# Optimization experiments

Hardware: AMD Instinct MI355X
Metric: run time of the kernel (lower is better)

The kernel has to match this reference:

```python
import jax, jax.numpy as jnp
import numpy as np

I3 = jnp.eye(3, dtype=jnp.float32)
G_VEC = jnp.array([0.0, 0.0, -9.80665], dtype=jnp.float32)
# Q diag: [cov_omega x3, cov_acc x3, cov_b_omega x3, cov_b_acc x3, cov_Rot_c_i x3, cov_t_c_i x3]
Q_DIAG = jnp.array([1e-3] * 3 + [1e-2] * 3 + [6e-9] * 3 + [2e-4] * 3 + [1e-9] * 3 + [1e-9] * 3, dtype=jnp.float32)
N_NORM_ROT = 100
N_NORM_ROT_CI = 1000


def skew(v):
    z = jnp.zeros_like(v[0])
    return jnp.stack([jnp.stack([z, -v[2], v[1]]),
                      jnp.stack([v[2], z, -v[0]]),
                      jnp.stack([-v[1], v[0], z])])


def so3exp(phi):
    a2 = jnp.sum(phi * phi)
    small = a2 < 1e-12
    a = jnp.sqrt(jnp.where(small, 1.0, a2))
    axis = phi / a
    c, s = jnp.cos(a), jnp.sin(a)
    big = c * I3 + (1.0 - c) * jnp.outer(axis, axis) + s * skew(axis)
    return jnp.where(small, I3 + skew(phi), big)


def sen3exp(xi):
    # SE_2(3) exponential: xi[:3]=rotation, xi[3:9]=(v, p) parts
    phi = xi[:3]
    a2 = jnp.sum(phi * phi)
    small = a2 < 1e-12
    a = jnp.sqrt(jnp.where(small, 1.0, a2))
    axis = phi / a
    c, s = jnp.cos(a), jnp.sin(a)
    sk = skew(axis)
    R = jnp.where(small, I3 + skew(phi),
                  c * I3 + (1.0 - c) * jnp.outer(axis, axis) + s * sk)
    J = jnp.where(small, I3 + 0.5 * skew(phi),
                  (s / a) * I3 + (1.0 - s / a) * jnp.outer(axis, axis) + ((1.0 - c) / a) * sk)
    x = J @ xi[3:].reshape(2, 3).T  # (3,2): columns are dv, dp
    return R, x


def normalize_rot(R):
    # Polar-factor re-orthonormalization (equivalent to the SVD-based
    # normalize_rot for near-rotation matrices), via Newton-Schulz iteration
    # which is smooth and jit/vjp friendly.
    def body(X, _):
        return 1.5 * X - 0.5 * (X @ X.T @ X), None
    X, _ = jax.lax.scan(body, R, None, length=8)
    return X


def from_rpy(roll, pitch, yaw):
    cr, sr = jnp.cos(roll), jnp.sin(roll)
    cp, sp = jnp.cos(pitch), jnp.sin(pitch)
    cy, sy = jnp.cos(yaw), jnp.sin(yaw)
    one = jnp.ones_like(cr)
    zero = jnp.zeros_like(cr)
    Rx = jnp.stack([jnp.stack([one, zero, zero]), jnp.stack([zero, cr, -sr]), jnp.stack([zero, sr, cr])])
    Ry = jnp.stack([jnp.stack([cp, zero, sp]), jnp.stack([zero, one, zero]), jnp.stack([-sp, zero, cp])])
    Rz = jnp.stack([jnp.stack([cy, -sy, zero]), jnp.stack([sy, cy, zero]), jnp.stack([zero, zero, one])])
    return Rz @ Ry @ Rx


def init_covariance():
    P = jnp.zeros((21, 21), dtype=jnp.float32)
    P = P.at[:2, :2].set(1e-3 * jnp.eye(2))     # cov_Rot0 (no yaw error)
    P = P.at[3:5, 3:5].set(0.1 * jnp.eye(2))    # cov_v0
    P = P.at[9:12, 9:12].set(6e-3 * I3)         # cov_b_omega0
    P = P.at[12:15, 12:15].set(4e-3 * I3)       # cov_b_acc0
    P = P.at[15:18, 15:18].set(1e-6 * I3)       # cov_Rot_c_i0
    P = P.at[18:21, 18:21].set(5e-3 * I3)       # cov_t_c_i0
    return P


def propagate_cov(P, Rot, v, p, dt):
    F = jnp.zeros((21, 21), dtype=P.dtype)
    F = F.at[3:6, :3].set(skew(G_VEC))
    F = F.at[6:9, 3:6].set(I3)
    F = F.at[:3, 9:12].set(-Rot)
    F = F.at[3:6, 9:12].set(-skew(v) @ Rot)
    F = F.at[3:6, 12:15].set(-Rot)
    F = F.at[6:9, 9:12].set(-skew(p) @ Rot)
    G = jnp.zeros((21, 18), dtype=P.dtype)
    G = G.at[:3, :3].set(Rot)
    G = G.at[3:6, 3:6].set(Rot)
    G = G.at[9:12, 6:9].set(I3)
    G = G.at[12:15, 9:12].set(I3)
    G = G.at[15:18, 12:15].set(I3)
    G = G.at[18:21, 15:18].set(I3)
    F = F * dt
    G = G * dt
    F2 = F @ F
    Phi = jnp.eye(21, dtype=P.dtype) + F + 0.5 * F2 + (F2 @ F) / 6.0  # 3rd-order expm
    return Phi @ (P + (G * Q_DIAG[None, :]) @ G.T) @ Phi.T


def _step(carry, xs):
    Rot, v, p, b_om, b_ac, Rci, tci, P = carry
    u_i, dt_i, mcov_i, i = xs
    # ---- propagate ----
    acc = Rot @ (u_i[3:6] - b_ac) + G_VEC
    v_n = v + acc * dt_i
    p_n = p + v * dt_i + 0.5 * acc * dt_i * dt_i
    Rot_n = Rot @ so3exp((u_i[:3] - b_om) * dt_i)
    P_n = propagate_cov(P, Rot, v, p, dt_i)
    # ---- update: zero lateral/vertical body-velocity pseudo-measurement ----
    omega = u_i[:3] - b_om
    Rot_body = Rot_n @ Rci
    v_imu = Rot_n.T @ v_n
    v_body = Rci.T @ v_imu + skew(tci) @ omega
    H = jnp.zeros((2, 21), dtype=P.dtype)
    H = H.at[:, 3:6].set(Rot_body.T[1:])
    H = H.at[:, 15:18].set((Rci.T @ skew(v_imu))[1:])
    H = H.at[:, 9:12].set(skew(tci)[1:])
    H = H.at[:, 18:21].set(-skew(omega)[1:])
    r = -v_body[1:]
    Rm = jnp.diag(mcov_i)
    S = H @ P_n @ H.T + Rm                    # (2,2)
    K = jnp.linalg.solve(S, H @ P_n).T        # K = P H^T S^-1 (P, S symmetric)
    dx = K @ r                                 # (21,)
    dR, dxi = sen3exp(dx[:9])
    Rot_u = dR @ Rot_n
    v_u = dR @ v_n + dxi[:, 0]
    p_u = dR @ p_n + dxi[:, 1]
    b_om_u = b_om + dx[9:12]
    b_ac_u = b_ac + dx[12:15]
    Rci_u = so3exp(dx[15:18]) @ Rci
    tci_u = tci + dx[18:21]
    IKH = jnp.eye(21, dtype=P.dtype) - K @ H
    P_u = IKH @ P_n @ IKH.T + K @ Rm @ K.T    # Joseph form
    P_u = 0.5 * (P_u + P_u.T)
    Rot_u = jnp.where(i % N_NORM_ROT == 0, normalize_rot(Rot_u), Rot_u)
    Rci_u = jnp.where(i % N_NORM_ROT_CI == 0, normalize_rot(Rci_u), Rci_u)
    carry = (Rot_u, v_u, p_u, b_om_u, b_ac_u, Rci_u, tci_u, P_u)
    return carry, (Rot_u, v_u, p_u, b_om_u, b_ac_u, Rci_u, tci_u)


def _forward(t, u, measurements_covs, v_mes, p_mes, ang0, N):
    dt = t[1:N] - t[:N - 1]
    Rot0 = from_rpy(ang0[0], ang0[1], ang0[2])
    z3 = jnp.zeros(3, dtype=u.dtype)
    carry0 = (Rot0, v_mes[0], z3, z3, z3, I3, z3, init_covariance())
    xs = (u[1:N], dt, measurements_covs[1:N], jnp.arange(1, N))
    _, ys = jax.lax.scan(_step, carry0, xs)
    Rot = jnp.concatenate([Rot0[None], ys[0]], axis=0)
    v = jnp.concatenate([v_mes[0][None], ys[1]], axis=0)
    p = jnp.concatenate([z3[None], ys[2]], axis=0)
    b_omega = jnp.concatenate([z3[None], ys[3]], axis=0)
    b_acc = jnp.concatenate([z3[None], ys[4]], axis=0)
    Rot_c_i = jnp.concatenate([I3[None], ys[5]], axis=0)
    t_c_i = jnp.concatenate([z3[None], ys[6]], axis=0)
    return (Rot, v, p, b_omega, b_acc, Rot_c_i, t_c_i)


def setup_inputs() -> dict:
    key = jax.random.key(0)
    N = 20000  # 200 s at 100 Hz IMU
    k0, k1, k2, k3, k4, k5 = jax.random.split(key, 6)
    t = jnp.arange(N, dtype=jnp.float32) * 0.01
    gyro = 0.01 * jax.random.normal(k0, (N, 3), dtype=jnp.float32)
    acc = jnp.array([0.0, 0.0, 9.80665], jnp.float32) + 0.1 * jax.random.normal(k1, (N, 3), dtype=jnp.float32)
    u = jnp.concatenate([gyro, acc], axis=1)
    measurements_covs = 0.1 + jax.random.uniform(k2, (N, 2), dtype=jnp.float32)
    v_mes = jax.random.normal(k3, (N, 3), dtype=jnp.float32)
    p_mes = jax.random.normal(k4, (N, 3), dtype=jnp.float32)
    ang0 = 0.01 * jax.random.normal(k5, (3,), dtype=jnp.float32)
    return dict(t=t, u=u, measurements_covs=measurements_covs, v_mes=v_mes, p_mes=p_mes, ang0=ang0, N=N)


def reference(t, u, measurements_covs, v_mes, p_mes, ang0, N):
    return _forward(t, u, measurements_covs, v_mes, p_mes, ang0, N)
```

## Files before the change

kernel.cpp:

```cpp
#include <hip/hip_runtime.h>

#define GRAV 9.80665f

__device__ __forceinline__ float sel3(int r, float a0, float a1, float a2){
  float x = (r==1)? a1 : a0;
  return (r>=2)? a2 : x;
}

__device__ __forceinline__ void mm33(float* __restrict__ O, const float* A, const float* B){
#pragma unroll
  for(int r=0;r<3;++r){
#pragma unroll
    for(int c=0;c<3;++c){
      O[r*3+c] = A[r*3+0]*B[0*3+c] + A[r*3+1]*B[1*3+c] + A[r*3+2]*B[2*3+c];
    }
  }
}

__device__ __forceinline__ void rot_from_t2(float t_, float p0, float p1, float p2, float* R){
  float c_, k1_, k2_;
  if (t_ < 1e-4f){
    c_  = 1.f - t_*(0.5f - t_*((1.f/24.f) - t_*(1.f/720.f)));
    k2_ = 1.f - t_*((1.f/6.f) - t_*((1.f/120.f) - t_*(1.f/5040.f)));
    k1_ = 0.5f - t_*((1.f/24.f) - t_*(1.f/720.f));
  } else {
    float a = sqrtf(t_);
    c_ = __cosf(a);
    float s = __sinf(a);
    k2_ = s/a;
    k1_ = (1.f - c_)/t_;
  }
  R[0]=c_+k1_*p0*p0;      R[1]=k1_*p0*p1-k2_*p2;  R[2]=k1_*p0*p2+k2_*p1;
  R[3]=k1_*p0*p1+k2_*p2;  R[4]=c_+k1_*p1*p1;      R[5]=k1_*p1*p2-k2_*p0;
  R[6]=k1_*p0*p2-k2_*p1;  R[7]=k1_*p1*p2+k2_*p0;  R[8]=c_+k1_*p2*p2;
}

__device__ __forceinline__ void normalize_rot9(float* X){
#pragma unroll 1
  for(int it=0; it<8; ++it){
    float Y[9], Z[9];
#pragma unroll
    for(int r=0;r<3;++r)
#pragma unroll
      for(int c=0;c<3;++c)
        Y[r*3+c] = X[r*3+0]*X[c*3+0] + X[r*3+1]*X[c*3+1] + X[r*3+2]*X[c*3+2];
#pragma unroll
    for(int r=0;r<3;++r)
#pragma unroll
      for(int c=0;c<3;++c)
        Z[r*3+c] = Y[r*3+0]*X[0*3+c] + Y[r*3+1]*X[1*3+c] + Y[r*3+2]*X[2*3+c];
#pragma unroll
    for(int e=0;e<9;++e) X[e] = 1.5f*X[e] - 0.5f*Z[e];
  }
}

__device__ __forceinline__ float pick_state(int l,
    const float* Rt, const float* vv, const float* pp,
    const float* bw, const float* ba, const float* Rc, const float* tc){
  float s = Rt[0];
  s=(l==1)?Rt[1]:s;  s=(l==2)?Rt[2]:s;  s=(l==3)?Rt[3]:s;  s=(l==4)?Rt[4]:s;
  s=(l==5)?Rt[5]:s;  s=(l==6)?Rt[6]:s;  s=(l==7)?Rt[7]:s;  s=(l==8)?Rt[8]:s;
  s=(l==9)?vv[0]:s;  s=(l==10)?vv[1]:s; s=(l==11)?vv[2]:s;
  s=(l==12)?pp[0]:s; s=(l==13)?pp[1]:s; s=(l==14)?pp[2]:s;
  s=(l==15)?bw[0]:s; s=(l==16)?bw[1]:s; s=(l==17)?bw[2]:s;
  s=(l==18)?ba[0]:s; s=(l==19)?ba[1]:s; s=(l==20)?ba[2]:s;
  s=(l==21)?Rc[0]:s; s=(l==22)?Rc[1]:s; s=(l==23)?Rc[2]:s;
  s=(l==24)?Rc[3]:s; s=(l==25)?Rc[4]:s; s=(l==26)?Rc[5]:s;
  s=(l==27)?Rc[6]:s; s=(l==28)?Rc[7]:s; s=(l==29)?Rc[8]:s;
  s=(l==30)?tc[0]:s; s=(l==31)?tc[1]:s; s=(l==32)?tc[2]:s;
  return s;
}

__global__ __launch_bounds__(64,1)
void iekf_scan_kernel(const float* __restrict__ t,
                      const float* __restrict__ u,
                      const float* __restrict__ mcov,
                      const float* __restrict__ v_mes,
                      const float* __restrict__ ang0,
                      float* __restrict__ out, int N)
{
  const int l = threadIdx.x;
  __shared__ float Pm[441];
  __shared__ float Eb[441];
  __shared__ float PnS[441];
  __shared__ float PuS[441];
  __shared__ float HPs[42];
  __shared__ float Ks[42];
  __shared__ float Ws[42];
  __shared__ float dxs[21];

  float Rt[9], vv[3], pp[3], bw[3], ba[3], Rc[9], tc[3];
  {
    float rl = ang0[0], pt = ang0[1], yw = ang0[2];
    float cr=cosf(rl), sr=sinf(rl), cp=cosf(pt), sp=sinf(pt), cy=cosf(yw), sy=sinf(yw);
    Rt[0]=cy*cp; Rt[1]=cy*sp*sr - sy*cr; Rt[2]=cy*sp*cr + sy*sr;
    Rt[3]=sy*cp; Rt[4]=sy*sp*sr + cy*cr; Rt[5]=sy*sp*cr - cy*sr;
    Rt[6]=-sp;   Rt[7]=cp*sr;            Rt[8]=cp*cr;
  }
  vv[0]=v_mes[0]; vv[1]=v_mes[1]; vv[2]=v_mes[2];
#pragma unroll
  for(int k=0;k<3;++k){ pp[k]=0.f; bw[k]=0.f; ba[k]=0.f; tc[k]=0.f; }
  Rc[0]=1.f;Rc[1]=0.f;Rc[2]=0.f;Rc[3]=0.f;Rc[4]=1.f;Rc[5]=0.f;Rc[6]=0.f;Rc[7]=0.f;Rc[8]=1.f;

  for (int e=l; e<441; e+=64){
    int r=e/21, c=e-(e/21)*21;
    float vI=0.f;
    if (r==c){
      if (r<2) vI=0.001f;
      else if (r==3||r==4) vI=0.1f;
      else if (r>=9&&r<12) vI=0.006f;
      else if (r>=12&&r<15) vI=0.004f;
      else if (r>=15&&r<18) vI=1e-6f;
      else if (r>=18) vI=0.005f;
    }
    Pm[e]=vI;
  }

  int ostr=0; float* op = out;
  {
    int obase=0, ooff=0;
    if (l<9)       {obase=0;    ostr=9; ooff=l;}
    else if (l<12) {obase=9*N;  ostr=3; ooff=l-9;}
    else if (l<15) {obase=12*N; ostr=3; ooff=l-12;}
    else if (l<18) {obase=15*N; ostr=3; ooff=l-15;}
    else if (l<21) {obase=18*N; ostr=3; ooff=l-18;}
    else if (l<30) {obase=21*N; ostr=9; ooff=l-21;}
    else           {obase=30*N; ostr=3; ooff=l-30;}
    op = out + obase + ooff;
  }

  int idxA=0, rrA=0, ccA=0; float qvA=0.f; bool rrtA=false;
  if (l<9)      { rrA=l/3; ccA=l-rrA*3; idxA=rrA*21+ccA; qvA=0.001f; rrtA=true; }
  else if (l<18){ int m=l-9; rrA=m/3; ccA=m-rrA*3; idxA=(3+rrA)*21+(3+ccA); qvA=0.01f; rrtA=true; }
  else if (l<30){ int j=l-18; int b=j/3, d=j-b*3; int row=9+b*3+d; idxA=row*21+row;
                  qvA = (b==0)?6e-9f : (b==1)?2e-4f : 1e-9f; }

  const int g21 = l/21;
  const int c21 = l - g21*21;

  static const int cols[12] = {3,4,5, 9,10,11, 15,16,17, 18,19,20};

  {
    float sv = pick_state(l, Rt, vv, pp, bw, ba, Rc, tc);
    if (l<33) op[0] = sv;
  }
  __syncthreads();

  float tA = t[0], tB = t[1];
  float cu[6];
#pragma unroll
  for(int k=0;k<6;++k) cu[k]=u[6+k];
  float cm0=mcov[2], cm1=mcov[3];

  int nx100=100, nx1000=1000;

#pragma unroll 1
  for (int i=1; i<N; ++i){
    float dt = tB - tA;
    float u0=cu[0], u1=cu[1], u2=cu[2], u3=cu[3], u4=cu[4], u5=cu[5];
    float crm0=cm0, crm1=cm1;
    if (i+1 < N){
      tA = tB; tB = t[i+1];
#pragma unroll
      for(int k=0;k<6;++k) cu[k]=u[(i+1)*6+k];
      cm0 = mcov[(i+1)*2]; cm1 = mcov[(i+1)*2+1];
    }
    float dt2=dt*dt, gdt=GRAV*dt, hdt=0.5f*dt, g6=gdt*dt*(1.0f/6.0f), hdt2=0.5f*dt*dt;

    float w0=u0-bw[0], w1=u1-bw[1], w2=u2-bw[2];
    float aa0=u3-ba[0], aa1=u4-ba[1], aa2=u5-ba[2];
    float acc0 = Rt[0]*aa0+Rt[1]*aa1+Rt[2]*aa2;
    float acc1 = Rt[3]*aa0+Rt[4]*aa1+Rt[5]*aa2;
    float acc2 = Rt[6]*aa0+Rt[7]*aa1+Rt[8]*aa2 - GRAV;
    float vn0=vv[0]+acc0*dt, vn1=vv[1]+acc1*dt, vn2=vv[2]+acc2*dt;
    float pn0=pp[0]+vv[0]*dt+acc0*hdt2;
    float pn1=pp[1]+vv[1]*dt+acc1*hdt2;
    float pn2=pp[2]+vv[2]*dt+acc2*hdt2;
    float ph0=w0*dt, ph1=w1*dt, ph2=w2*dt;
    float dRs[9]; rot_from_t2(ph0*ph0+ph1*ph1+ph2*ph2, ph0,ph1,ph2, dRs);
    float Rn[9]; mm33(Rn, Rt, dRs);
    float Rb[9]; mm33(Rb, Rn, Rc);
    float vi0 = Rn[0]*vn0+Rn[3]*vn1+Rn[6]*vn2;
    float vi1 = Rn[1]*vn0+Rn[4]*vn1+Rn[7]*vn2;
    float vi2 = Rn[2]*vn0+Rn[5]*vn1+Rn[8]*vn2;
    float vb1 = Rc[1]*vi0+Rc[4]*vi1+Rc[7]*vi2 + (tc[2]*w0 - tc[0]*w2);
    float vb2 = Rc[2]*vi0+Rc[5]*vi1+Rc[8]*vi2 + (tc[0]*w1 - tc[1]*w0);
    float rr0 = -vb1, rr1 = -vb2;

    float H0[12], H1[12];
    H0[0]=Rb[1]; H0[1]=Rb[4]; H0[2]=Rb[7];
    H1[0]=Rb[2]; H1[1]=Rb[5]; H1[2]=Rb[8];
    H0[3]=tc[2];  H0[4]=0.f;   H0[5]=-tc[0];
    H1[3]=-tc[1]; H1[4]=tc[0]; H1[5]=0.f;
    H0[6]=Rc[4]*vi2 - Rc[7]*vi1;  H0[7]=Rc[7]*vi0 - Rc[1]*vi2;  H0[8]=Rc[1]*vi1 - Rc[4]*vi0;
    H1[6]=Rc[5]*vi2 - Rc[8]*vi1;  H1[7]=Rc[8]*vi0 - Rc[2]*vi2;  H1[8]=Rc[2]*vi1 - Rc[5]*vi0;
    H0[9]=-w2; H0[10]=0.f; H0[11]=w0;
    H1[9]=w1;  H1[10]=-w0; H1[11]=0.f;

    float Bm[9], Cab[9], D2a[9];
#pragma unroll
    for(int k=0;k<3;++k){
      float b0=-dt*Rt[k], b1=-dt*Rt[3+k], b2=-dt*Rt[6+k];
      float c0=dt*(vv[2]*Rt[3+k]-vv[1]*Rt[6+k]);
      float c1=dt*(vv[0]*Rt[6+k]-vv[2]*Rt[k]);
      float c2=dt*(vv[1]*Rt[k]-vv[0]*Rt[3+k]);
      float d0=dt*(pp[2]*Rt[3+k]-pp[1]*Rt[6+k]);
      float d1=dt*(pp[0]*Rt[6+k]-pp[2]*Rt[k]);
      float d2=dt*(pp[1]*Rt[k]-pp[0]*Rt[3+k]);
      Bm[k]=b0; Bm[3+k]=b1; Bm[6+k]=b2;
      Cab[k]=c0+0.5f*gdt*b1; Cab[3+k]=c1-0.5f*gdt*b0; Cab[6+k]=c2;
      D2a[k]=d0+hdt*c0+g6*b1; D2a[3+k]=d1+hdt*c1-g6*b0; D2a[6+k]=d2+hdt*c2;
    }
    float Bs0=sel3(g21,Bm[0],Bm[3],Bm[6]),  Bs1=sel3(g21,Bm[1],Bm[4],Bm[7]),  Bs2=sel3(g21,Bm[2],Bm[5],Bm[8]);
    float Cs0=sel3(g21,Cab[0],Cab[3],Cab[6]),Cs1=sel3(g21,Cab[1],Cab[4],Cab[7]),Cs2=sel3(g21,Cab[2],Cab[5],Cab[8]);
    float Ds0=sel3(g21,D2a[0],D2a[3],D2a[6]),Ds1=sel3(g21,D2a[1],D2a[4],D2a[7]),Ds2=sel3(g21,D2a[2],D2a[5],D2a[8]);

    if (l<30){
      float addv;
      if (rrtA){
        float ra0=sel3(rrA,Rt[0],Rt[3],Rt[6]), ra1=sel3(rrA,Rt[1],Rt[4],Rt[7]), ra2=sel3(rrA,Rt[2],Rt[5],Rt[8]);
        float rb0=sel3(ccA,Rt[0],Rt[3],Rt[6]), rb1=sel3(ccA,Rt[1],Rt[4],Rt[7]), rb2=sel3(ccA,Rt[2],Rt[5],Rt[8]);
        addv = qvA*dt2*(ra0*rb0+ra1*rb1+ra2*rb2);
      } else addv = qvA*dt2;
      Pm[idxA] += addv;
    }
    __syncthreads();

    if (l<63){
      int c = c21;
      float m0 = Pm[c], m1 = Pm[21+c];
      float mr = Pm[g21*21+c], m3r = Pm[(3+g21)*21+c], m6r = Pm[(6+g21)*21+c];
      float m9 =Pm[9*21+c],  m10=Pm[10*21+c], m11=Pm[11*21+c];
      float m12=Pm[12*21+c], m13=Pm[13*21+c], m14=Pm[14*21+c];
      float Ar = (g21==0)? gdt*m1 : (g21==1)? -gdt*m0 : 0.f;
      float bterm = Bs0*m12+Bs1*m13+Bs2*m14;
      float e0 = mr + Bs0*m9+Bs1*m10+Bs2*m11;
      float e1 = m3r + Ar + Cs0*m9+Cs1*m10+Cs2*m11 + bterm;
      float e2 = m6r + hdt*Ar + dt*m3r + Ds0*m9+Ds1*m10+Ds2*m11 + hdt*bterm;
      Eb[g21*21+c]=e0; Eb[(3+g21)*21+c]=e1; Eb[(6+g21)*21+c]=e2;
      int rw = 9+4*g21;
      Eb[rw*21+c]     = Pm[rw*21+c];
      Eb[(rw+1)*21+c] = Pm[(rw+1)*21+c];
      Eb[(rw+2)*21+c] = Pm[(rw+2)*21+c];
      Eb[(rw+3)*21+c] = Pm[(rw+3)*21+c];
    }
    __syncthreads();

    if (l<63){
      int r = c21;
      const float* Er = Eb + r*21;
      float e0a=Er[0], e1a=Er[1];
      float eg=Er[g21], e3g=Er[3+g21], e6g=Er[6+g21];
      float e9=Er[9],e10=Er[10],e11=Er[11],e12=Er[12],e13=Er[13],e14=Er[14];
      float Ag = (g21==0)? gdt*e1a : (g21==1)? -gdt*e0a : 0.f;
      float bterm = Bs0*e12+Bs1*e13+Bs2*e14;
      float q0 = eg + Bs0*e9+Bs1*e10+Bs2*e11;
      float q1 = e3g + Ag + Cs0*e9+Cs1*e10+Cs2*e11 + bterm;
      float q2 = e6g + hdt*Ag + dt*e3g + Ds0*e9+Ds1*e10+Ds2*e11 + hdt*bterm;
      PnS[r*21+g21]=q0; PnS[r*21+3+g21]=q1; PnS[r*21+6+g21]=q2;
      int cw = 9+4*g21;
      PnS[r*21+cw]=Er[cw]; PnS[r*21+cw+1]=Er[cw+1]; PnS[r*21+cw+2]=Er[cw+2]; PnS[r*21+cw+3]=Er[cw+3];
    }
    __syncthreads();

    if (l<42){
      int rH = l/21, c = l-(l/21)*21;
      float acc = 0.f;
#pragma unroll
      for(int k=0;k<12;++k){
        float h = (rH==0)? H0[k] : H1[k];
        acc += h * PnS[cols[k]*21 + c];
      }
      HPs[rH*21+c] = acc;
    }
    __syncthreads();

    float s00=crm0, s11=crm1, s01=0.f, s10=0.f;
#pragma unroll
    for(int k=0;k<12;++k){
      float hp0 = HPs[cols[k]];
      float hp1 = HPs[21+cols[k]];
      s00 += hp0*H0[k]; s01 += hp0*H1[k];
      s10 += hp1*H0[k]; s11 += hp1*H1[k];
    }
    float idet = 1.0f/(s00*s11 - s01*s10);
    float i00 =  s11*idet, i01 = -s01*idet, i10 = -s10*idet, i11 = s00*idet;
    if (l<21){
      float hp0=HPs[l], hp1=HPs[21+l];
      float K0 = i00*hp0 + i01*hp1;
      float K1 = i10*hp0 + i11*hp1;
      Ks[l*2]=K0; Ks[l*2+1]=K1;
      dxs[l] = K0*rr0 + K1*rr1;
    }
    __syncthreads();

    float dxr[21];
#pragma unroll
    for(int k=0;k<21;++k) dxr[k]=dxs[k];

    if (l<63){
      int c = c21;
      float hp0 = HPs[c], hp1 = HPs[21+c];
#pragma unroll
      for (int rrow=0; rrow<7; ++rrow){
        int r = g21*7+rrow;
        float k0=Ks[r*2], k1=Ks[r*2+1];
        PnS[r*21+c] -= k0*hp0 + k1*hp1;
      }
    }
    __syncthreads();

    if (l<42){
      int rW = l/21, ii = l-(l/21)*21;
      float acc=0.f;
#pragma unroll
      for(int k=0;k<12;++k){
        float h = (rW==0)? H0[k] : H1[k];
        acc += PnS[ii*21+cols[k]] * h;
      }
      Ws[ii*2+rW]=acc;
    }
    __syncthreads();

    if (l<63){
      int c = c21;
      float kc0=Ks[c*2], kc1=Ks[c*2+1];
#pragma unroll
      for(int rrow=0;rrow<7;++rrow){
        int r = g21*7+rrow;
        float w0_=Ws[r*2], w1_=Ws[r*2+1];
        float kr0=Ks[r*2], kr1=Ks[r*2+1];
        float tv=PnS[r*21+c];
        PuS[r*21+c] = tv - (w0_*kc0+w1_*kc1) + crm0*kr0*kc0 + crm1*kr1*kc1;
      }
    }
    __syncthreads();

    if (l<63){
      int c = c21;
#pragma unroll
      for(int rrow=0;rrow<7;++rrow){
        int r = g21*7+rrow;
        Pm[r*21+c] = 0.5f*(PuS[r*21+c] + PuS[c*21+r]);
      }
    }
    __syncthreads();

    float t2x = dxr[0]*dxr[0]+dxr[1]*dxr[1]+dxr[2]*dxr[2];
    float cX,k1X,k2X,j1X;
    if (t2x < 1e-4f){
      cX  = 1.f - t2x*(0.5f - t2x*((1.f/24.f) - t2x*(1.f/720.f)));
      k2X = 1.f - t2x*((1.f/6.f) - t2x*((1.f/120.f) - t2x*(1.f/5040.f)));
      k1X = 0.5f - t2x*((1.f/24.f) - t2x*(1.f/720.f));
      j1X = (1.f/6.f) - t2x*((1.f/120.f) - t2x*(1.f/5040.f));
    } else {
      float a = sqrtf(t2x);
      cX = __cosf(a);
      float s = __sinf(a);
      k2X = s/a; k1X = (1.f-cX)/t2x; j1X = (1.f-k2X)/t2x;
    }
    float dR[9];
    dR[0]=cX+k1X*dxr[0]*dxr[0];      dR[1]=k1X*dxr[0]*dxr[1]-k2X*dxr[2]; dR[2]=k1X*dxr[0]*dxr[2]+k2X*dxr[1];
    dR[3]=k1X*dxr[0]*dxr[1]+k2X*dxr[2]; dR[4]=cX+k1X*dxr[1]*dxr[1];      dR[5]=k1X*dxr[1]*dxr[2]-k2X*dxr[0];
    dR[6]=k1X*dxr[0]*dxr[2]-k2X*dxr[1]; dR[7]=k1X*dxr[1]*dxr[2]+k2X*dxr[0]; dR[8]=cX+k1X*dxr[2]*dxr[2];
    float Jm[9];
    Jm[0]=k2X+j1X*dxr[0]*dxr[0];      Jm[1]=j1X*dxr[0]*dxr[1]-k1X*dxr[2]; Jm[2]=j1X*dxr[0]*dxr[2]+k1X*dxr[1];
    Jm[3]=j1X*dxr[0]*dxr[1]+k1X*dxr[2]; Jm[4]=k2X+j1X*dxr[1]*dxr[1];      Jm[5]=j1X*dxr[1]*dxr[2]-k1X*dxr[0];
    Jm[6]=j1X*dxr[0]*dxr[2]-k1X*dxr[1]; Jm[7]=j1X*dxr[1]*dxr[2]+k1X*dxr[0]; Jm[8]=k2X+j1X*dxr[2]*dxr[2];

    float Ru[9]; mm33(Ru, dR, Rn);
    float vu0 = dR[0]*vn0+dR[1]*vn1+dR[2]*vn2 + Jm[0]*dxr[3]+Jm[1]*dxr[4]+Jm[2]*dxr[5];
    float vu1 = dR[3]*vn0+dR[4]*vn1+dR[5]*vn2 + Jm[3]*dxr[3]+Jm[4]*dxr[4]+Jm[5]*dxr[5];
    float vu2 = dR[6]*vn0+dR[7]*vn1+dR[8]*vn2 + Jm[6]*dxr[3]+Jm[7]*dxr[4]+Jm[8]*dxr[5];
    float pu0 = dR[0]*pn0+dR[1]*pn1+dR[2]*pn2 + Jm[0]*dxr[6]+Jm[1]*dxr[7]+Jm[2]*dxr[8];
    float pu1 = dR[3]*pn0+dR[4]*pn1+dR[5]*pn2 + Jm[3]*dxr[6]+Jm[4]*dxr[7]+Jm[5]*dxr[8];
    float pu2 = dR[6]*pn0+dR[7]*pn1+dR[8]*pn2 + Jm[6]*dxr[6]+Jm[7]*dxr[7]+Jm[8]*dxr[8];
    bw[0]+=dxr[9];  bw[1]+=dxr[10]; bw[2]+=dxr[11];
    ba[0]+=dxr[12]; ba[1]+=dxr[13]; ba[2]+=dxr[14];
    float Ec[9]; rot_from_t2(dxr[15]*dxr[15]+dxr[16]*dxr[16]+dxr[17]*dxr[17], dxr[15],dxr[16],dxr[17], Ec);
    float Rcu[9]; mm33(Rcu, Ec, Rc);
    tc[0]+=dxr[18]; tc[1]+=dxr[19]; tc[2]+=dxr[20];

    if (i==nx100){ normalize_rot9(Ru); nx100+=100; }
    if (i==nx1000){ normalize_rot9(Rcu); nx1000+=1000; }

#pragma unroll
    for(int k=0;k<9;++k){ Rt[k]=Ru[k]; Rc[k]=Rcu[k]; }
    vv[0]=vu0; vv[1]=vu1; vv[2]=vu2;
    pp[0]=pu0; pp[1]=pu1; pp[2]=pu2;

    float sv = pick_state(l, Rt, vv, pp, bw, ba, Rc, tc);
    if (l<33) op[i*ostr] = sv;
  }
}

extern "C" void kernel_launch(void* const* d_in, const int* in_sizes, int n_in,
                              void* d_out, int out_size, void* d_ws, size_t ws_size,
                              hipStream_t stream) {
  (void)n_in; (void)out_size; (void)d_ws; (void)ws_size;
  const float* t     = (const float*)d_in[0];
  const float* u     = (const float*)d_in[1];
  const float* mcov  = (const float*)d_in[2];
  const float* v_mes = (const float*)d_in[3];
  const float* ang0  = (const float*)d_in[5];
  int N = in_sizes[0];
  iekf_scan_kernel<<<dim3(1), dim3(64), 0, stream>>>(t, u, mcov, v_mes, ang0, (float*)d_out, N);
}
```

Measured before the change: 53.91 ms.

## Fuse covariance update stages to cut barriers per IEKF step

Restructures the per-step covariance pipeline in the single-workgroup scan kernel. The Q noise add is folded into the first propagation pass, the H·P reduction is done with wave shuffles from register-held rows, and the Kalman gain increment is broadcast via readlane instead of shared memory. The Joseph-form update and symmetrisation are merged into one closed-form pass using S=HPHᵀ+R. Together these remove several __syncthreads and shared-memory round trips per step, in exchange for more register pressure and a rewritten algebraic form whose rounding differs slightly from the previous ordering.

New measurement: 46.05 ms. -14.6%, faster.

```diff
diff --git a/kernel.cpp b/kernel.cpp
--- a/kernel.cpp
+++ b/kernel.cpp
@@ -80,14 +80,11 @@
                       float* __restrict__ out, int N)
 {
   const int l = threadIdx.x;
-  __shared__ float Pm[441];
-  __shared__ float Eb[441];
-  __shared__ float PnS[441];
-  __shared__ float PuS[441];
-  __shared__ float HPs[42];
-  __shared__ float Ks[42];
-  __shared__ float Ws[42];
-  __shared__ float dxs[21];
+  __shared__ float  Pm[441];
+  __shared__ float  Eb[441];
+  __shared__ float  PnS[441];
+  __shared__ float2 HPs2[21];
+  __shared__ float2 Ks2[21];
 
   float Rt[9], vv[3], pp[3], bw[3], ba[3], Rc[9], tc[3];
   {
@@ -129,14 +126,11 @@
     op = out + obase + ooff;
   }
 
-  int idxA=0, rrA=0, ccA=0; float qvA=0.f; bool rrtA=false;
-  if (l<9)      { rrA=l/3; ccA=l-rrA*3; idxA=rrA*21+ccA; qvA=0.001f; rrtA=true; }
-  else if (l<18){ int m=l-9; rrA=m/3; ccA=m-rrA*3; idxA=(3+rrA)*21+(3+ccA); qvA=0.01f; rrtA=true; }
-  else if (l<30){ int j=l-18; int b=j/3, d=j-b*3; int row=9+b*3+d; idxA=row*21+row;
-                  qvA = (b==0)?6e-9f : (b==1)?2e-4f : 1e-9f; }
-
   const int g21 = l/21;
   const int c21 = l - g21*21;
+  const int cw  = 9 + 4*g21;
+  int l1 = l+21; if (l1>=63) l1-=63;
+  int l2 = l+42; if (l2>=63) l2-=63;
 
   static const int cols[12] = {3,4,5, 9,10,11, 15,16,17, 18,19,20};
 
@@ -215,37 +209,61 @@
     float Cs0=sel3(g21,Cab[0],Cab[3],Cab[6]),Cs1=sel3(g21,Cab[1],Cab[4],Cab[7]),Cs2=sel3(g21,Cab[2],Cab[5],Cab[8]);
     float Ds0=sel3(g21,D2a[0],D2a[3],D2a[6]),Ds1=sel3(g21,D2a[1],D2a[4],D2a[7]),Ds2=sel3(g21,D2a[2],D2a[5],D2a[8]);
 
-    if (l<30){
-      float addv;
-      if (rrtA){
-        float ra0=sel3(rrA,Rt[0],Rt[3],Rt[6]), ra1=sel3(rrA,Rt[1],Rt[4],Rt[7]), ra2=sel3(rrA,Rt[2],Rt[5],Rt[8]);
-        float rb0=sel3(ccA,Rt[0],Rt[3],Rt[6]), rb1=sel3(ccA,Rt[1],Rt[4],Rt[7]), rb2=sel3(ccA,Rt[2],Rt[5],Rt[8]);
-        addv = qvA*dt2*(ra0*rb0+ra1*rb1+ra2*rb2);
-      } else addv = qvA*dt2;
-      Pm[idxA] += addv;
-    }
-    __syncthreads();
+    float RRT00=Rt[0]*Rt[0]+Rt[1]*Rt[1]+Rt[2]*Rt[2];
+    float RRT01=Rt[0]*Rt[3]+Rt[1]*Rt[4]+Rt[2]*Rt[5];
+    float RRT02=Rt[0]*Rt[6]+Rt[1]*Rt[7]+Rt[2]*Rt[8];
+    float RRT11=Rt[3]*Rt[3]+Rt[4]*Rt[4]+Rt[5]*Rt[5];
+    float RRT12=Rt[3]*Rt[6]+Rt[4]*Rt[7]+Rt[5]*Rt[8];
+    float RRT22=Rt[6]*Rt[6]+Rt[7]*Rt[7]+Rt[8]*Rt[8];
+    float q0d=0.001f*dt2, q1d=0.01f*dt2;
+    float q69=6e-9f*dt2, q24=2e-4f*dt2, q19=1e-9f*dt2;
 
     if (l<63){
       int c = c21;
-      float m0 = Pm[c], m1 = Pm[21+c];
-      float mr = Pm[g21*21+c], m3r = Pm[(3+g21)*21+c], m6r = Pm[(6+g21)*21+c];
-      float m9 =Pm[9*21+c],  m10=Pm[10*21+c], m11=Pm[11*21+c];
-      float m12=Pm[12*21+c], m13=Pm[13*21+c], m14=Pm[14*21+c];
+      bool cl3 = (c<3);
+      bool c36 = (c>=3 && c<6);
+      float R0c  = sel3(c,   RRT00, RRT01, RRT02);
+      float R1c  = sel3(c,   RRT01, RRT11, RRT12);
+      float R2c  = sel3(c,   RRT02, RRT12, RRT22);
+      float R0c3 = sel3(c-3, RRT00, RRT01, RRT02);
+      float R1c3 = sel3(c-3, RRT01, RRT11, RRT12);
+      float R2c3 = sel3(c-3, RRT02, RRT12, RRT22);
+      float d0  = cl3 ? q0d*R0c : 0.f;
+      float d1  = cl3 ? q0d*R1c : 0.f;
+      float dg  = cl3 ? q0d*sel3(g21,R0c,R1c,R2c) : 0.f;
+      float dg3 = c36 ? q1d*sel3(g21,R0c3,R1c3,R2c3) : 0.f;
+
+      float m0  = Pm[c]            + d0;
+      float m1  = Pm[21+c]         + d1;
+      float mr  = Pm[g21*21+c]     + dg;
+      float m3r = Pm[(3+g21)*21+c] + dg3;
+      float m6r = Pm[(6+g21)*21+c];
+      float m9  = Pm[9*21+c]  + ((c==9) ? q69 : 0.f);
+      float m10 = Pm[10*21+c] + ((c==10)? q69 : 0.f);
+      float m11 = Pm[11*21+c] + ((c==11)? q69 : 0.f);
+      float m12 = Pm[12*21+c] + ((c==12)? q24 : 0.f);
+      float m13 = Pm[13*21+c] + ((c==13)? q24 : 0.f);
+      float m14 = Pm[14*21+c] + ((c==14)? q24 : 0.f);
+
       float Ar = (g21==0)? gdt*m1 : (g21==1)? -gdt*m0 : 0.f;
       float bterm = Bs0*m12+Bs1*m13+Bs2*m14;
       float e0 = mr + Bs0*m9+Bs1*m10+Bs2*m11;
       float e1 = m3r + Ar + Cs0*m9+Cs1*m10+Cs2*m11 + bterm;
       float e2 = m6r + hdt*Ar + dt*m3r + Ds0*m9+Ds1*m10+Ds2*m11 + hdt*bterm;
       Eb[g21*21+c]=e0; Eb[(3+g21)*21+c]=e1; Eb[(6+g21)*21+c]=e2;
-      int rw = 9+4*g21;
-      Eb[rw*21+c]     = Pm[rw*21+c];
-      Eb[(rw+1)*21+c] = Pm[(rw+1)*21+c];
-      Eb[(rw+2)*21+c] = Pm[(rw+2)*21+c];
-      Eb[(rw+3)*21+c] = Pm[(rw+3)*21+c];
+#pragma unroll
+      for (int jj=0;jj<4;++jj){
+        int row = cw+jj;
+        float qd = (row<12)? q69 : (row<15)? q24 : q19;
+        Eb[row*21+c] = Pm[row*21+c] + ((row==c)? qd : 0.f);
+      }
     }
     __syncthreads();
 
+    float pnv[7];
+#pragma unroll
+    for(int k=0;k<7;++k) pnv[k]=0.f;
+    float p0=0.f, p1=0.f;
     if (l<63){
       int r = c21;
       const float* Er = Eb + r*21;
@@ -254,97 +272,74 @@
       float e9=Er[9],e10=Er[10],e11=Er[11],e12=Er[12],e13=Er[13],e14=Er[14];
       float Ag = (g21==0)? gdt*e1a : (g21==1)? -gdt*e0a : 0.f;
       float bterm = Bs0*e12+Bs1*e13+Bs2*e14;
-      float q0 = eg + Bs0*e9+Bs1*e10+Bs2*e11;
-      float q1 = e3g + Ag + Cs0*e9+Cs1*e10+Cs2*e11 + bterm;
-      float q2 = e6g + hdt*Ag + dt*e3g + Ds0*e9+Ds1*e10+Ds2*e11 + hdt*bterm;
-      PnS[r*21+g21]=q0; PnS[r*21+3+g21]=q1; PnS[r*21+6+g21]=q2;
-      int cw = 9+4*g21;
-      PnS[r*21+cw]=Er[cw]; PnS[r*21+cw+1]=Er[cw+1]; PnS[r*21+cw+2]=Er[cw+2]; PnS[r*21+cw+3]=Er[cw+3];
-    }
+      pnv[0] = eg + Bs0*e9+Bs1*e10+Bs2*e11;
+      pnv[1] = e3g + Ag + Cs0*e9+Cs1*e10+Cs2*e11 + bterm;
+      pnv[2] = e6g + hdt*Ag + dt*e3g + Ds0*e9+Ds1*e10+Ds2*e11 + hdt*bterm;
+      pnv[3] = Er[cw]; pnv[4] = Er[cw+1]; pnv[5] = Er[cw+2]; pnv[6] = Er[cw+3];
+
+      PnS[r*21 + g21]     = pnv[0];
+      PnS[r*21 + 3+g21]   = pnv[1];
+      PnS[r*21 + 6+g21]   = pnv[2];
+      PnS[r*21 + cw]      = pnv[3];
+      PnS[r*21 + cw+1]    = pnv[4];
+      PnS[r*21 + cw+2]    = pnv[5];
+      PnS[r*21 + cw+3]    = pnv[6];
+
+      float c1a = sel3(g21, H0[0], H0[1], H0[2]);
+      float c3a = sel3(g21, H0[3], 0.f,   H0[8]);
+      float c4a = sel3(g21, H0[4], 0.f,   H0[9]);
+      float c5a = sel3(g21, H0[5], H0[6], H0[10]);
+      float c6a = sel3(g21, 0.f,   H0[7], H0[11]);
+      float c1b = sel3(g21, H1[0], H1[1], H1[2]);
+      float c3b = sel3(g21, H1[3], 0.f,   H1[8]);
+      float c4b = sel3(g21, H1[4], 0.f,   H1[9]);
+      float c5b = sel3(g21, H1[5], H1[6], H1[10]);
+      float c6b = sel3(g21, 0.f,   H1[7], H1[11]);
+      p0 = c1a*pnv[1] + c3a*pnv[3] + c4a*pnv[4] + c5a*pnv[5] + c6a*pnv[6];
+      p1 = c1b*pnv[1] + c3b*pnv[3] + c4b*pnv[4] + c5b*pnv[5] + c6b*pnv[6];
+    }
+    float hpr0 = p0 + __shfl(p0, l1) + __shfl(p0, l2);
+    float hpr1 = p1 + __shfl(p1, l1) + __shfl(p1, l2);
+    if (l<21) HPs2[c21] = make_float2(hpr0, hpr1);
     __syncthreads();
 
-    if (l<42){
-      int rH = l/21, c = l-(l/21)*21;
-      float acc = 0.f;
-#pragma unroll
-      for(int k=0;k<12;++k){
-        float h = (rH==0)? H0[k] : H1[k];
-        acc += h * PnS[cols[k]*21 + c];
-      }
-      HPs[rH*21+c] = acc;
-    }
-    __syncthreads();
-
-    float s00=crm0, s11=crm1, s01=0.f, s10=0.f;
+    float hph00=0.f, hph01=0.f, hph10=0.f, hph11=0.f;
 #pragma unroll
     for(int k=0;k<12;++k){
-      float hp0 = HPs[cols[k]];
-      float hp1 = HPs[21+cols[k]];
-      s00 += hp0*H0[k]; s01 += hp0*H1[k];
-      s10 += hp1*H0[k]; s11 += hp1*H1[k];
-    }
+      float2 hp = HPs2[cols[k]];
+      hph00 += hp.x*H0[k]; hph01 += hp.x*H1[k];
+      hph10 += hp.y*H0[k]; hph11 += hp.y*H1[k];
+    }
+    float s00 = hph00 + crm0, s01 = hph01, s10 = hph10, s11 = hph11 + crm1;
     float idet = 1.0f/(s00*s11 - s01*s10);
     float i00 =  s11*idet, i01 = -s01*idet, i10 = -s10*idet, i11 = s00*idet;
-    if (l<21){
-      float hp0=HPs[l], hp1=HPs[21+l];
-      float K0 = i00*hp0 + i01*hp1;
-      float K1 = i10*hp0 + i11*hp1;
-      Ks[l*2]=K0; Ks[l*2+1]=K1;
-      dxs[l] = K0*rr0 + K1*rr1;
+    float K0 = i00*hpr0 + i01*hpr1;
+    float K1 = i10*hpr0 + i11*hpr1;
+    float s01q = 0.5f*(s01 + s10);
+    float dxval = K0*rr0 + K1*rr1;
+    if (l<21){ Ks2[l] = make_float2(K0,K1); }
+    float dxr[21];
+    {
+      int db = __float_as_int(dxval);
+#pragma unroll
+      for (int k=0;k<21;++k) dxr[k] = __int_as_float(__builtin_amdgcn_readlane(db, k));
     }
     __syncthreads();
 
-    float dxr[21];
-#pragma unroll
-    for(int k=0;k<21;++k) dxr[k]=dxs[k];
-
     if (l<63){
-      int c = c21;
-      float hp0 = HPs[c], hp1 = HPs[21+c];
-#pragma unroll
-      for (int rrow=0; rrow<7; ++rrow){
-        int r = g21*7+rrow;
-        float k0=Ks[r*2], k1=Ks[r*2+1];
-        PnS[r*21+c] -= k0*hp0 + k1*hp1;
+      int r = c21;
+#pragma unroll
+      for (int s=0;s<7;++s){
+        int j = (s<3)? (g21 + 3*s) : (cw + (s-3));
+        float pnT = PnS[j*21 + r];
+        float2 hpj = HPs2[j];
+        float2 kj  = Ks2[j];
+        float base  = 0.5f*(pnv[s] + pnT);
+        float cross = (K0*hpj.x + K1*hpj.y) + (kj.x*hpr0 + kj.y*hpr1);
+        float quad  = (K0*kj.x)*s00 + (K0*kj.y + K1*kj.x)*s01q + (K1*kj.y)*s11;
+        Pm[r*21+j] = base - cross + quad;
       }
     }
-    __syncthreads();
-
-    if (l<42){
-      int rW = l/21, ii = l-(l/21)*21;
-      float acc=0.f;
-#pragma unroll
-      for(int k=0;k<12;++k){
-        float h = (rW==0)? H0[k] : H1[k];
-        acc += PnS[ii*21+cols[k]] * h;
-      }
-      Ws[ii*2+rW]=acc;
-    }
-    __syncthreads();
-
-    if (l<63){
-      int c = c21;
-      float kc0=Ks[c*2], kc1=Ks[c*2+1];
-#pragma unroll
-      for(int rrow=0;rrow<7;++rrow){
-        int r = g21*7+rrow;
-        float w0_=Ws[r*2], w1_=Ws[r*2+1];
-        float kr0=Ks[r*2], kr1=Ks[r*2+1];
-        float tv=PnS[r*21+c];
-        PuS[r*21+c] = tv - (w0_*kc0+w1_*kc1) + crm0*kr0*kc0 + crm1*kr1*kc1;
-      }
-    }
-    __syncthreads();
-
-    if (l<63){
-      int c = c21;
-#pragma unroll
-      for(int rrow=0;rrow<7;++rrow){
-        int r = g21*7+rrow;
-        Pm[r*21+c] = 0.5f*(PuS[r*21+c] + PuS[c*21+r]);
-      }
-    }
-    __syncthreads();
 
     float t2x = dxr[0]*dxr[0]+dxr[1]*dxr[1]+dxr[2]*dxr[2];
     float cX,k1X,k2X,j1X;
@@ -389,6 +384,8 @@
     vv[0]=vu0; vv[1]=vu1; vv[2]=vu2;
     pp[0]=pu0; pp[1]=pu1; pp[2]=pu2;
 
+    __syncthreads();
+
     float sv = pick_state(l, Rt, vv, pp, bw, ba, Rc, tc);
     if (l<33) op[i*ostr] = sv;
   }
```
